# Optimization experiments

Hardware: AMD Instinct MI355X
Metric: run time of the kernel (lower is better)

The kernel has to match this reference:

```python
import jax, jax.numpy as jnp
import numpy as np

N_NODES = 50000
N_EDGES = 800000
D = 128


def setup_inputs() -> dict:
    key = jax.random.key(0)
    ks = jax.random.split(key, 8)
    scale = 1.0 / np.sqrt(D)
    x = jax.random.normal(ks[0], (N_NODES, D), dtype=jnp.float32)
    edge_index = jax.random.randint(ks[1], (2, N_EDGES), 0, N_NODES, dtype=jnp.int64)
    return {
        "x": x,
        "edge_index": edge_index,
        "w1_l": jax.random.normal(ks[2], (D, D), dtype=jnp.float32) * scale,
        "w1_r": jax.random.normal(ks[3], (D, D), dtype=jnp.float32) * scale,
        "b1": jnp.zeros((D,), dtype=jnp.float32),
        "w2_l": jax.random.normal(ks[4], (D, D), dtype=jnp.float32) * scale,
        "w2_r": jax.random.normal(ks[5], (D, D), dtype=jnp.float32) * scale,
        "b2": jnp.zeros((D,), dtype=jnp.float32),
    }


def _sage_conv(x, src, dst, w_l, w_r, b):
    # mean aggregation of source features at destination nodes
    n = x.shape[0]
    msg = x[src]                                            # [E, D] gather
    agg = jax.ops.segment_sum(msg, dst, num_segments=n)      # [N, D] scatter-add
    cnt = jax.ops.segment_sum(jnp.ones((src.shape[0],), x.dtype), dst, num_segments=n)
    mean = agg / jnp.maximum(cnt, 1.0)[:, None]
    # out = lin_l(mean_agg) + lin_r(x) + bias  (PyG SAGEConv default)
    return mean @ w_l.T + x @ w_r.T + b


def reference(x, edge_index, w1_l, w1_r, b1, w2_l, w2_r, b2):
    src, dst = edge_index[0], edge_index[1]
    h = jax.nn.relu(_sage_conv(x, src, dst, w1_l, w1_r, b1))
    out = _sage_conv(h, src, dst, w2_l, w2_r, b2)
    return out
```

## Files before the change

### kernel.cpp

```cpp
#include <hip/hip_runtime.h>

#define D 128
#define CAP 48
#define TILE 32

typedef unsigned short u16;
typedef unsigned int u32;
typedef _Float16 f16;
typedef __attribute__((ext_vector_type(4))) _Float16 h4;
typedef __attribute__((ext_vector_type(8))) _Float16 h8;
typedef __attribute__((ext_vector_type(4))) float f32x4;

__global__ __launch_bounds__(256) void mega_prep(const float* __restrict__ x,
                                                 f16* __restrict__ xh, int n8,
                                                 const float* __restrict__ w1l,
                                                 const float* __restrict__ w1r,
                                                 const float* __restrict__ w2l,
                                                 const float* __restrict__ w2r,
                                                 f16* __restrict__ wb1,
                                                 f16* __restrict__ wb2,
                                                 const int* __restrict__ src,
                                                 const int* __restrict__ dst,
                                                 int* __restrict__ cnt,
                                                 int* __restrict__ edge_pad,
                                                 int E, int bucketDiv, int perChunk,
                                                 int cvtBlocks, int wBlocks) {
    const int b = blockIdx.x;
    const int t = threadIdx.x;
    if (b < cvtBlocks) {
        int i = b * 256 + t;
        if (i < n8) {
            float4 v0 = reinterpret_cast<const float4*>(x)[2 * i];
            float4 v1 = reinterpret_cast<const float4*>(x)[2 * i + 1];
            h8 o;
            o[0] = (f16)v0.x; o[1] = (f16)v0.y; o[2] = (f16)v0.z; o[3] = (f16)v0.w;
            o[4] = (f16)v1.x; o[5] = (f16)v1.y; o[6] = (f16)v1.z; o[7] = (f16)v1.w;
            reinterpret_cast<h8*>(xh)[i] = o;
        }
    } else if (b < cvtBlocks + wBlocks) {
        int e = (b - cvtBlocks) * 256 + t;
        int which = e >> 15;
        int i = e & 32767;
        int j = i >> 8, k = i & 255;
        const float* wl = which ? w2l : w1l;
        const float* wr = which ? w2r : w1r;
        f16* wb = which ? wb2 : wb1;
        float v = (k < 128) ? wl[j * 128 + k] : wr[j * 128 + k - 128];
        wb[i] = (f16)v;
    } else {
        const int fillIdx = b - cvtBlocks - wBlocks;
        const int bucket = b & 7;
        const int chunk = fillIdx >> 3;
        const int lo = bucket * bucketDiv;
        const int hi = lo + bucketDiv;
        const int beg = chunk * perChunk;
        const int end = min(E, beg + perChunk);
        for (int base = beg + t * 4; base < end; base += 1024) {
            if (base + 3 < end) {
                int4 d = *reinterpret_cast<const int4*>(dst + base);
                if (d.x >= lo && d.x < hi) { int p = atomicAdd(&cnt[d.x], 1); if (p < CAP) edge_pad[d.x * CAP + p] = src[base + 0]; }
                if (d.y >= lo && d.y < hi) { int p = atomicAdd(&cnt[d.y], 1); if (p < CAP) edge_pad[d.y * CAP + p] = src[base + 1]; }
                if (d.z >= lo && d.z < hi) { int p = atomicAdd(&cnt[d.z], 1); if (p < CAP) edge_pad[d.z * CAP + p] = src[base + 2]; }
                if (d.w >= lo && d.w < hi) { int p = atomicAdd(&cnt[d.w], 1); if (p < CAP) edge_pad[d.w * CAP + p] = src[base + 3]; }
            } else {
                for (int j = 0; j < 4 && base + j < end; ++j) {
                    int d = dst[base + j];
                    if (d >= lo && d < hi) { int p = atomicAdd(&cnt[d], 1); if (p < CAP) edge_pad[d * CAP + p] = src[base + j]; }
                }
            }
        }
    }
}

template <int RELU, int OUTF16>
__global__ __launch_bounds__(256) void sage_fused(const f16* __restrict__ feat,
                                                  const int* __restrict__ cnt,
                                                  const int* __restrict__ edge_pad,
                                                  const f16* __restrict__ wb,
                                                  const float* __restrict__ bias,
                                                  float* __restrict__ outf,
                                                  f16* __restrict__ outh, int n) {
    __shared__ f16 sM[TILE * 128];
    __shared__ int eLds[TILE * CAP];
    __shared__ int degLds[TILE];
    const int t = threadIdx.x;
    const int base = blockIdx.x * TILE;
    char* sMb = reinterpret_cast<char*>(sM);

    {
        const int4* gseg = reinterpret_cast<const int4*>(edge_pad + (size_t)base * CAP);
#pragma unroll
        for (int i = 0; i < (TILE * CAP / 4 + 255) / 256; ++i) {
            int idx = i * 256 + t;
            if (idx < TILE * CAP / 4) reinterpret_cast<int4*>(eLds)[idx] = gseg[idx];
        }
        if (t < TILE) degLds[t] = (base + t < n) ? cnt[base + t] : 0;
    }
    __syncthreads();

    {
        const int halfId = t >> 5;
        const int lane = t & 31;
#pragma unroll
        for (int rnd = 0; rnd < TILE / 8; ++rnd) {
            const int nl = rnd * 8 + halfId;
            const int deg = degLds[nl];
            const int stored = min(deg, CAP);
            const int* ep = &eLds[nl * CAP];

            h4 acc = (h4){0, 0, 0, 0};
            int j = 0;
            for (; j + 8 <= stored; j += 8) {
                int4 ia = *reinterpret_cast<const int4*>(ep + j);
                int4 ib = *reinterpret_cast<const int4*>(ep + j + 4);
                h4 v0 = *reinterpret_cast<const h4*>(feat + (size_t)ia.x * D + lane * 4);
                h4 v1 = *reinterpret_cast<const h4*>(feat + (size_t)ia.y * D + lane * 4);
                h4 v2 = *reinterpret_cast<const h4*>(feat + (size_t)ia.z * D + lane * 4);
                h4 v3 = *reinterpret_cast<const h4*>(feat + (size_t)ia.w * D + lane * 4);
                h4 v4 = *reinterpret_cast<const h4*>(feat + (size_t)ib.x * D + lane * 4);
                h4 v5 = *reinterpret_cast<const h4*>(feat + (size_t)ib.y * D + lane * 4);
                h4 v6 = *reinterpret_cast<const h4*>(feat + (size_t)ib.z * D + lane * 4);
                h4 v7 = *reinterpret_cast<const h4*>(feat + (size_t)ib.w * D + lane * 4);
                acc += ((v0 + v1) + (v2 + v3)) + ((v4 + v5) + (v6 + v7));
            }
            for (; j + 4 <= stored; j += 4) {
                int4 ia = *reinterpret_cast<const int4*>(ep + j);
                h4 v0 = *reinterpret_cast<const h4*>(feat + (size_t)ia.x * D + lane * 4);
                h4 v1 = *reinterpret_cast<const h4*>(feat + (size_t)ia.y * D + lane * 4);
                h4 v2 = *reinterpret_cast<const h4*>(feat + (size_t)ia.z * D + lane * 4);
                h4 v3 = *reinterpret_cast<const h4*>(feat + (size_t)ia.w * D + lane * 4);
                acc += (v0 + v1) + (v2 + v3);
            }
            for (; j < stored; ++j) {
                int s = ep[j];
                acc += *reinterpret_cast<const h4*>(feat + (size_t)s * D + lane * 4);
            }

            const f16 sc = (deg > 0) ? (f16)(1.f / (float)deg) : (f16)0;
            h4 o = acc * (h4){sc, sc, sc, sc};
            int lin = nl * 256 + lane * 8;
            *reinterpret_cast<h4*>(sMb + (lin ^ ((nl & 7) << 4))) = o;
        }
    }
    __syncthreads();

    const int wid = t >> 6, lane = t & 63;
    const int l15 = lane & 15, l4 = lane >> 4;
    const int colBase = wid * 32;

    int rowA[2];
#pragma unroll
    for (int m = 0; m < 2; ++m) {
        int r = base + m * 16 + l15;
        rowA[m] = (r < n) ? r : 0;
    }

    f32x4 acc2[2][2];
#pragma unroll
    for (int m = 0; m < 2; ++m)
#pragma unroll
        for (int q = 0; q < 2; ++q) acc2[m][q] = (f32x4){0.f, 0.f, 0.f, 0.f};

    const int swr = (l15 & 7) << 4;

#pragma unroll
    for (int ks = 0; ks < 8; ++ks) {
        h8 afr[2];
        if (ks < 4) {
#pragma unroll
            for (int m = 0; m < 2; ++m) {
                int lin = (m * 16 + l15) * 256 + ks * 64 + l4 * 16;
                afr[m] = *reinterpret_cast<const h8*>(sMb + (lin ^ swr));
            }
        } else {
            const int kk = (ks & 3) * 32 + l4 * 8;
#pragma unroll
            for (int m = 0; m < 2; ++m)
                afr[m] = *reinterpret_cast<const h8*>(feat + (size_t)rowA[m] * D + kk);
        }
#pragma unroll
        for (int q = 0; q < 2; ++q) {
            h8 bfr = *reinterpret_cast<const h8*>(
                wb + (size_t)(colBase + q * 16 + l15) * 256 + ks * 32 + l4 * 8);
#pragma unroll
            for (int m = 0; m < 2; ++m)
                acc2[m][q] = __builtin_amdgcn_mfma_f32_16x16x32_f16(afr[m], bfr, acc2[m][q], 0, 0, 0);
        }
    }

#pragma unroll
    for (int q = 0; q < 2; ++q) {
        const int col = colBase + q * 16 + l15;
        const float bv = bias[col];
#pragma unroll
        for (int m = 0; m < 2; ++m) {
#pragma unroll
            for (int r = 0; r < 4; ++r) {
                int orow = base + m * 16 + l4 * 4 + r;
                if (orow < n) {
                    float v = acc2[m][q][r] + bv;
                    if (RELU) v = fmaxf(v, 0.f);
                    if (OUTF16)
                        outh[(size_t)orow * D + col] = (f16)v;
                    else
                        outf[(size_t)orow * D + col] = v;
                }
            }
        }
    }
}

extern "C" void kernel_launch(void* const* d_in, const int* in_sizes, int n_in,
                              void* d_out, int out_size, void* d_ws, size_t ws_size,
                              hipStream_t stream) {
    const float* x   = (const float*)d_in[0];
    const int*   ei  = (const int*)d_in[1];
    const float* w1l = (const float*)d_in[2];
    const float* w1r = (const float*)d_in[3];
    const float* b1  = (const float*)d_in[4];
    const float* w2l = (const float*)d_in[5];
    const float* w2r = (const float*)d_in[6];
    const float* b2  = (const float*)d_in[7];
    float* out = (float*)d_out;

    const int N = in_sizes[0] / D;
    const int E = in_sizes[1] / 2;

    const int* src = ei;
    const int* dst = ei + E;

    const int gridFused = (N + TILE - 1) / TILE;
    const int Nceil = gridFused * TILE;

    char* ws = (char*)d_ws;
    auto align = [](size_t v) { return (v + 255) & ~(size_t)255; };
    const size_t featB = align((size_t)N * D * sizeof(f16));

    f16* xh       = (f16*)ws;   ws += featB;
    f16* hh       = (f16*)ws;   ws += featB;
    f16* wb1      = (f16*)ws;   ws += align(128 * 256 * sizeof(f16));
    f16* wb2      = (f16*)ws;   ws += align(128 * 256 * sizeof(f16));
    int* cnt      = (int*)ws;   ws += align((size_t)Nceil * sizeof(int));
    int* edge_pad = (int*)ws;   ws += align((size_t)Nceil * CAP * sizeof(int));

    const int n8        = N * D / 8;
    const int cvtBlocks = (n8 + 255) / 256;
    const int wBlocks   = 256;
    const int bucketDiv = (N + 7) / 8;
    const int perChunk  = 5120;
    const int chunks    = (E + perChunk - 1) / perChunk;
    const int fillBlocks = 8 * chunks;

    hipMemsetAsync(cnt, 0, (size_t)Nceil * sizeof(int), stream);
    mega_prep<<<cvtBlocks + wBlocks + fillBlocks, 256, 0, stream>>>(
        x, xh, n8, w1l, w1r, w2l, w2r, wb1, wb2,
        src, dst, cnt, edge_pad, E, bucketDiv, perChunk, cvtBlocks, wBlocks);

    sage_fused<1, 1><<<gridFused, 256, 0, stream>>>(xh, cnt, edge_pad, wb1, b1, nullptr, hh, N);

    sage_fused<0, 0><<<gridFused, 256, 0, stream>>>(hh, cnt, edge_pad, wb2, b2, out, nullptr, N);
}
```

Before: 152.6 us.

## Bin edges into per-bucket queues before CSR fill; stage outputs through LDS

Edge bucketing now runs in two passes. Each block reads every edge once, bins it by destination range into eight global queues using shared-memory counters, and a second kernel replays each queue to do the per-node atomic fill. Previously every edge chunk was read eight times, once per bucket. Separately, the fused SAGE kernel writes its results through shared memory so that global stores are coalesced vector rows instead of scattered scalar writes. This adds a kernel launch, extra queue traffic, and float-based bucket math that could misbin nodes near range boundaries.

```diff
diff --git a/kernel.cpp b/kernel.cpp
--- a/kernel.cpp
+++ b/kernel.cpp
@@ -4,27 +4,25 @@
 #define CAP 48
 #define TILE 32
 
-typedef unsigned short u16;
-typedef unsigned int u32;
 typedef _Float16 f16;
 typedef __attribute__((ext_vector_type(4))) _Float16 h4;
 typedef __attribute__((ext_vector_type(8))) _Float16 h8;
 typedef __attribute__((ext_vector_type(4))) float f32x4;
 
-__global__ __launch_bounds__(256) void mega_prep(const float* __restrict__ x,
-                                                 f16* __restrict__ xh, int n8,
-                                                 const float* __restrict__ w1l,
-                                                 const float* __restrict__ w1r,
-                                                 const float* __restrict__ w2l,
-                                                 const float* __restrict__ w2r,
-                                                 f16* __restrict__ wb1,
-                                                 f16* __restrict__ wb2,
-                                                 const int* __restrict__ src,
-                                                 const int* __restrict__ dst,
-                                                 int* __restrict__ cnt,
-                                                 int* __restrict__ edge_pad,
-                                                 int E, int bucketDiv, int perChunk,
-                                                 int cvtBlocks, int wBlocks) {
+__global__ __launch_bounds__(256) void prep_bin(const float* __restrict__ x,
+                                                f16* __restrict__ xh, int n8,
+                                                const float* __restrict__ w1l,
+                                                const float* __restrict__ w1r,
+                                                const float* __restrict__ w2l,
+                                                const float* __restrict__ w2r,
+                                                f16* __restrict__ wb1,
+                                                f16* __restrict__ wb2,
+                                                const int* __restrict__ src,
+                                                const int* __restrict__ dst,
+                                                int E, int2* __restrict__ queue,
+                                                int* __restrict__ qTail, int qcap,
+                                                float invDiv,
+                                                int cvtBlocks, int wBlocks) {
     const int b = blockIdx.x;
     const int t = threadIdx.x;
     if (b < cvtBlocks) {
@@ -48,27 +46,65 @@
         float v = (k < 128) ? wl[j * 128 + k] : wr[j * 128 + k - 128];
         wb[i] = (f16)v;
     } else {
-        const int fillIdx = b - cvtBlocks - wBlocks;
-        const int bucket = b & 7;
-        const int chunk = fillIdx >> 3;
-        const int lo = bucket * bucketDiv;
-        const int hi = lo + bucketDiv;
-        const int beg = chunk * perChunk;
-        const int end = min(E, beg + perChunk);
-        for (int base = beg + t * 4; base < end; base += 1024) {
-            if (base + 3 < end) {
-                int4 d = *reinterpret_cast<const int4*>(dst + base);
-                if (d.x >= lo && d.x < hi) { int p = atomicAdd(&cnt[d.x], 1); if (p < CAP) edge_pad[d.x * CAP + p] = src[base + 0]; }
-                if (d.y >= lo && d.y < hi) { int p = atomicAdd(&cnt[d.y], 1); if (p < CAP) edge_pad[d.y * CAP + p] = src[base + 1]; }
-                if (d.z >= lo && d.z < hi) { int p = atomicAdd(&cnt[d.z], 1); if (p < CAP) edge_pad[d.z * CAP + p] = src[base + 2]; }
-                if (d.w >= lo && d.w < hi) { int p = atomicAdd(&cnt[d.w], 1); if (p < CAP) edge_pad[d.w * CAP + p] = src[base + 3]; }
+        __shared__ int binCnt[8];
+        __shared__ int binBase[8];
+        const int chunk = b - cvtBlocks - wBlocks;
+        const int beg = chunk * 4096;
+        const int end = min(E, beg + 4096);
+        if (t < 8) binCnt[t] = 0;
+        __syncthreads();
+
+        int4 dv[4], sv[4];
+#pragma unroll
+        for (int i = 0; i < 4; ++i) {
+            int a = beg + i * 1024 + t * 4;
+            dv[i] = make_int4(-1, -1, -1, -1);
+            sv[i] = make_int4(0, 0, 0, 0);
+            if (a + 3 < end) {
+                dv[i] = *reinterpret_cast<const int4*>(dst + a);
+                sv[i] = *reinterpret_cast<const int4*>(src + a);
             } else {
-                for (int j = 0; j < 4 && base + j < end; ++j) {
-                    int d = dst[base + j];
-                    if (d >= lo && d < hi) { int p = atomicAdd(&cnt[d], 1); if (p < CAP) edge_pad[d * CAP + p] = src[base + j]; }
-                }
-            }
-        }
+                if (a + 0 < end) { dv[i].x = dst[a + 0]; sv[i].x = src[a + 0]; }
+                if (a + 1 < end) { dv[i].y = dst[a + 1]; sv[i].y = src[a + 1]; }
+                if (a + 2 < end) { dv[i].z = dst[a + 2]; sv[i].z = src[a + 2]; }
+                if (a + 3 < end) { dv[i].w = dst[a + 3]; sv[i].w = src[a + 3]; }
+            }
+        }
+        auto bkt = [&](int d) { return min(7, (int)(((float)d + 0.5f) * invDiv)); };
+        auto cnt1 = [&](int d) { if (d >= 0) atomicAdd(&binCnt[bkt(d)], 1); };
+#pragma unroll
+        for (int i = 0; i < 4; ++i) { cnt1(dv[i].x); cnt1(dv[i].y); cnt1(dv[i].z); cnt1(dv[i].w); }
+        __syncthreads();
+        if (t < 8) { binBase[t] = atomicAdd(&qTail[t], binCnt[t]); binCnt[t] = 0; }
+        __syncthreads();
+        auto place = [&](int d, int s) {
+            if (d >= 0) {
+                int bk = bkt(d);
+                int pos = binBase[bk] + atomicAdd(&binCnt[bk], 1);
+                if (pos < qcap) queue[(size_t)bk * qcap + pos] = make_int2(d, s);
+            }
+        };
+#pragma unroll
+        for (int i = 0; i < 4; ++i) {
+            place(dv[i].x, sv[i].x); place(dv[i].y, sv[i].y);
+            place(dv[i].z, sv[i].z); place(dv[i].w, sv[i].w);
+        }
+    }
+}
+
+__global__ __launch_bounds__(256) void fill_queue(const int2* __restrict__ queue,
+                                                  const int* __restrict__ qTail,
+                                                  int* __restrict__ cnt,
+                                                  int* __restrict__ edge_pad,
+                                                  int qcap, int gB) {
+    const int b = blockIdx.x & 7;
+    const int slice = blockIdx.x >> 3;
+    const int total = min(qTail[b], qcap);
+    const int2* q = queue + (size_t)b * qcap;
+    for (int i = slice * 256 + threadIdx.x; i < total; i += gB * 256) {
+        int2 p = q[i];
+        int pos = atomicAdd(&cnt[p.x], 1);
+        if (pos < CAP) edge_pad[(size_t)p.x * CAP + pos] = p.y;
     }
 }
 
@@ -80,12 +116,12 @@
                                                   const float* __restrict__ bias,
                                                   float* __restrict__ outf,
                                                   f16* __restrict__ outh, int n) {
-    __shared__ f16 sM[TILE * 128];
-    __shared__ int eLds[TILE * CAP];
-    __shared__ int degLds[TILE];
+    __shared__ float4 smemRaw4[1024];
+    char* sMb   = reinterpret_cast<char*>(smemRaw4);
+    int*  eLds  = reinterpret_cast<int*>(sMb + 8192);
+    int*  degLds= reinterpret_cast<int*>(sMb + 8192 + 6144);
     const int t = threadIdx.x;
     const int base = blockIdx.x * TILE;
-    char* sMb = reinterpret_cast<char*>(sM);
 
     {
         const int4* gseg = reinterpret_cast<const int4*>(edge_pad + (size_t)base * CAP);
@@ -188,24 +224,56 @@
         }
     }
 
-#pragma unroll
-    for (int q = 0; q < 2; ++q) {
-        const int col = colBase + q * 16 + l15;
-        const float bv = bias[col];
-#pragma unroll
-        for (int m = 0; m < 2; ++m) {
-#pragma unroll
-            for (int r = 0; r < 4; ++r) {
-                int orow = base + m * 16 + l4 * 4 + r;
-                if (orow < n) {
+    __syncthreads();
+    if (OUTF16) {
+        f16* oT = reinterpret_cast<f16*>(sMb);
+#pragma unroll
+        for (int q = 0; q < 2; ++q) {
+            const int col = colBase + q * 16 + l15;
+            const float bv = bias[col];
+#pragma unroll
+            for (int m = 0; m < 2; ++m)
+#pragma unroll
+                for (int r = 0; r < 4; ++r) {
                     float v = acc2[m][q][r] + bv;
                     if (RELU) v = fmaxf(v, 0.f);
-                    if (OUTF16)
-                        outh[(size_t)orow * D + col] = (f16)v;
-                    else
-                        outf[(size_t)orow * D + col] = v;
+                    oT[(m * 16 + l4 * 4 + r) * 128 + col] = (f16)v;
                 }
-            }
+        }
+        __syncthreads();
+#pragma unroll
+        for (int it = 0; it < 2; ++it) {
+            int idx = it * 256 + t;
+            int row = idx >> 4;
+            int c = (idx & 15) * 8;
+            if (base + row < n)
+                *reinterpret_cast<h8*>(outh + (size_t)(base + row) * D + c) =
+                    *reinterpret_cast<const h8*>(oT + row * 128 + c);
+        }
+    } else {
+        float* oT = reinterpret_cast<float*>(sMb);
+#pragma unroll
+        for (int q = 0; q < 2; ++q) {
+            const int col = colBase + q * 16 + l15;
+            const float bv = bias[col];
+#pragma unroll
+            for (int m = 0; m < 2; ++m)
+#pragma unroll
+                for (int r = 0; r < 4; ++r) {
+                    float v = acc2[m][q][r] + bv;
+                    if (RELU) v = fmaxf(v, 0.f);
+                    oT[(m * 16 + l4 * 4 + r) * 128 + col] = v;
+                }
+        }
+        __syncthreads();
+#pragma unroll
+        for (int it = 0; it < 4; ++it) {
+            int idx = it * 256 + t;
+            int row = idx >> 5;
+            int c = (idx & 31) * 4;
+            if (base + row < n)
+                *reinterpret_cast<float4*>(outf + (size_t)(base + row) * D + c) =
+                    *reinterpret_cast<const float4*>(oT + row * 128 + c);
         }
     }
 }
@@ -235,26 +303,30 @@
     char* ws = (char*)d_ws;
     auto align = [](size_t v) { return (v + 255) & ~(size_t)255; };
     const size_t featB = align((size_t)N * D * sizeof(f16));
+    const int qcap = ((E / 4) + 1023) & ~1023;
 
     f16* xh       = (f16*)ws;   ws += featB;
     f16* hh       = (f16*)ws;   ws += featB;
     f16* wb1      = (f16*)ws;   ws += align(128 * 256 * sizeof(f16));
     f16* wb2      = (f16*)ws;   ws += align(128 * 256 * sizeof(f16));
-    int* cnt      = (int*)ws;   ws += align((size_t)Nceil * sizeof(int));
+    int* cnt      = (int*)ws;   ws += align(((size_t)Nceil + 8) * sizeof(int));
+    int* qTail    = cnt + Nceil;
     int* edge_pad = (int*)ws;   ws += align((size_t)Nceil * CAP * sizeof(int));
+    int2* queue   = (int2*)ws;  ws += align((size_t)8 * qcap * sizeof(int2));
 
     const int n8        = N * D / 8;
     const int cvtBlocks = (n8 + 255) / 256;
     const int wBlocks   = 256;
-    const int bucketDiv = (N + 7) / 8;
-    const int perChunk  = 5120;
-    const int chunks    = (E + perChunk - 1) / perChunk;
-    const int fillBlocks = 8 * chunks;
-
-    hipMemsetAsync(cnt, 0, (size_t)Nceil * sizeof(int), stream);
-    mega_prep<<<cvtBlocks + wBlocks + fillBlocks, 256, 0, stream>>>(
+    const int binBlocks = (E + 4095) / 4096;
+    const int bucketDiv = (Nceil + 7) / 8;
+    const float invDiv  = 1.0f / (float)bucketDiv;
+    const int gB        = 64;
+
+    hipMemsetAsync(cnt, 0, ((size_t)Nceil + 8) * sizeof(int), stream);
+    prep_bin<<<cvtBlocks + wBlocks + binBlocks, 256, 0, stream>>>(
         x, xh, n8, w1l, w1r, w2l, w2r, wb1, wb2,
-        src, dst, cnt, edge_pad, E, bucketDiv, perChunk, cvtBlocks, wBlocks);
+        src, dst, E, queue, qTail, qcap, invDiv, cvtBlocks, wBlocks);
+    fill_queue<<<8 * gB, 256, 0, stream>>>(queue, qTail, cnt, edge_pad, qcap, gB);
 
     sage_fused<1, 1><<<gridFused, 256, 0, stream>>>(xh, cnt, edge_pad, wb1, b1, nullptr, hh, N);
 
```

Result: no change. 151.9 us (-0.4%).
